# Kernel tuning notes

Measured on AMD Instinct MI355X. Metric: run time of the kernel, lower is better.

Reference implementation:

```python
import jax, jax.numpy as jnp
import numpy as np

B, N, E = 2, 16384, 262144          # batch, nodes, directed edges (avg deg 16)
K, D, Wm = 256, 3, 1                # nmodes, ndims, nmeasures
C, L, FC = 128, 4, 128              # channels, Fourier layers, fc hidden
IN_DIM, OUT_DIM = 3, 1


def setup_inputs() -> dict:
    key = jax.random.key(0)
    ks = jax.random.split(key, 20)
    s = 1.0 / (C * C)
    inp = {
        "x": jax.random.normal(ks[0], (B, N, IN_DIM), jnp.float32),
        "nodes": jax.random.uniform(ks[1], (B, N, D), jnp.float32),
        "node_mask": jnp.ones((B, N, 1), jnp.float32),
        "node_weights": jax.random.uniform(ks[2], (B, N, Wm), jnp.float32) / N,
        "directed_edges": jax.random.randint(ks[3], (B, E, 2), 0, N),
        "edge_gradient_weights": jax.random.normal(ks[4], (B, E, D), jnp.float32),
        "modes": jax.random.normal(ks[5], (K, D, Wm), jnp.float32),
        "sp_L": jnp.ones((D, Wm), jnp.float32),
        "weights_c": s * jax.random.uniform(ks[6], (L, C, C, K, Wm), jnp.float32),
        "weights_s": s * jax.random.uniform(ks[7], (L, C, C, K, Wm), jnp.float32),
        "weights_0": s * jax.random.uniform(ks[8], (L, C, C, 1, Wm), jnp.float32),
        "fc0_w": jax.random.normal(ks[9], (C, IN_DIM), jnp.float32) * 0.1,
        "fc0_b": jnp.zeros((C,), jnp.float32),
        "ws_w": jax.random.normal(ks[10], (L, C, C), jnp.float32) * 0.05,
        "ws_b": jnp.zeros((L, C), jnp.float32),
        "gws_w": jax.random.normal(ks[11], (L, C, D * C), jnp.float32) * 0.05,
        "gws_b": jnp.zeros((L, C), jnp.float32),
        "fc1_w": jax.random.normal(ks[12], (FC, C), jnp.float32) * 0.05,
        "fc1_b": jnp.zeros((FC,), jnp.float32),
        "fc2_w": jax.random.normal(ks[13], (OUT_DIM, FC), jnp.float32) * 0.05,
        "fc2_b": jnp.zeros((OUT_DIM,), jnp.float32),
    }
    return inp


def _gelu(x):
    return jax.nn.gelu(x, approximate=False)  # torch F.gelu default = exact erf


def _compute_gradient(f, directed_edges, edge_gradient_weights):
    # f: [B, C, N] -> gradients [B, C*D, N] via directed-edge scatter-add
    fT = jnp.transpose(f, (0, 2, 1))                       # [B, N, C]
    tgt, src = directed_edges[..., 0], directed_edges[..., 1]
    f_src = jnp.take_along_axis(fT, src[..., None], axis=1)  # [B, E, C]
    f_tgt = jnp.take_along_axis(fT, tgt[..., None], axis=1)
    msg = jnp.einsum('bed,bec->becd', edge_gradient_weights, f_src - f_tgt)
    msg = msg.reshape(msg.shape[0], msg.shape[1], -1)        # [B, E, C*D]

    def scat(m, t):
        return jnp.zeros((fT.shape[1], m.shape[-1]), m.dtype).at[t].add(m)

    g = jax.vmap(scat)(msg, tgt)                             # [B, N, C*D]
    return jnp.transpose(g, (0, 2, 1))


def _spectral_conv(x, wc, wsn, w0, bc, bs, b0, wbc, wbs, wb0):
    # x: [B, C_in, N]
    xc = jnp.einsum('bix,bxkw->bikw', x, wbc)
    xs = -jnp.einsum('bix,bxkw->bikw', x, wbs)
    x0 = jnp.einsum('bix,bxkw->bikw', x, wb0)
    fc = jnp.einsum('bikw,iokw->bokw', xc, wc) - jnp.einsum('bikw,iokw->bokw', xs, wsn)
    fs = jnp.einsum('bikw,iokw->bokw', xs, wc) + jnp.einsum('bikw,iokw->bokw', xc, wsn)
    f0 = jnp.einsum('bikw,iokw->bokw', x0, w0)
    return (jnp.einsum('bokw,bxkw->box', f0, b0)
            + 2.0 * jnp.einsum('bokw,bxkw->box', fc, bc)
            - 2.0 * jnp.einsum('bokw,bxkw->box', fs, bs))


def reference(x, nodes, node_mask, node_weights, directed_edges, edge_gradient_weights,
              modes, sp_L, weights_c, weights_s, weights_0,
              fc0_w, fc0_b, ws_w, ws_b, gws_w, gws_b, fc1_w, fc1_b, fc2_w, fc2_b):
    # Fourier bases with learnable length-scale sp_L: [K,D,Wm]*[D,Wm]
    temp = jnp.einsum('bxd,kdw->bxkw', nodes, modes * sp_L)   # [B,N,K,Wm]
    bc, bs = jnp.cos(temp), jnp.sin(temp)
    b0 = jnp.zeros((temp.shape[0], temp.shape[1], 1, temp.shape[3]), temp.dtype)
    nw = (node_weights * node_mask)[:, :, None, :]            # [B,N,1,Wm]
    wbc, wbs, wb0 = bc * nw, bs * nw, b0 * nw

    h = jnp.einsum('bxi,ci->bxc', x, fc0_w) + fc0_b           # lift [B,N,C]
    h = jnp.transpose(h, (0, 2, 1))                           # [B,C,N]

    for i in range(L):
        x1 = _spectral_conv(h, weights_c[i], weights_s[i], weights_0[i],
                            bc, bs, b0, wbc, wbs, wb0)
        x2 = jnp.einsum('oc,bcn->bon', ws_w[i], h) + ws_b[i][None, :, None]
        grad = _compute_gradient(h, directed_edges, edge_gradient_weights)
        x3 = jnp.einsum('og,bgn->bon', gws_w[i], grad) + gws_b[i][None, :, None]
        h = x1 + x2 + x3
        if i != L - 1:
            h = _gelu(h)

    h = jnp.transpose(h, (0, 2, 1))                           # [B,N,C]
    h = _gelu(jnp.einsum('bnc,fc->bnf', h, fc1_w) + fc1_b)
    out = jnp.einsum('bnf,of->bno', h, fc2_w) + fc2_b         # [B,N,out_dim]
    return out
```

## Files before the change

kernel.cpp:

```cpp
#include <hip/hip_runtime.h>
#include <math.h>

#define Bn 2
#define Nn 16384
#define En 262144
#define Kn 256
#define Cn 128
#define Rn 512
#define Ln 4
#define LDP 72
#define NSPLIT 64
#define MMSPLIT 4

typedef float f32x4 __attribute__((ext_vector_type(4)));
typedef short s16x8 __attribute__((ext_vector_type(8)));

__device__ __forceinline__ float gelu_f(float x){
  return 0.5f*x*(1.0f + erff(x*0.70710678118654752440f));
}
__device__ __forceinline__ unsigned short f2b(float x){
  unsigned int u = __float_as_uint(x);
  unsigned int r = (u + 0x7FFFu + ((u>>16)&1u)) >> 16;
  return (unsigned short)r;
}
__device__ __forceinline__ float b2f(unsigned short h){
  return __uint_as_float(((unsigned int)h)<<16);
}
__device__ __forceinline__ unsigned int pack2(float lo, float hi){
  return (unsigned int)f2b(lo) | ((unsigned int)f2b(hi) << 16);
}


__global__ __launch_bounds__(256) void k_nw(const float* __restrict__ nwt,
                                            const float* __restrict__ msk,
                                            float* __restrict__ nw){
  int i = blockIdx.x*256 + threadIdx.x;
  nw[i] = nwt[i]*msk[i];
}

__global__ __launch_bounds__(256) void k_basis(const float* __restrict__ nodes,
                                               const float* __restrict__ modes,
                                               const float* __restrict__ spl,
                                               unsigned short* __restrict__ basis,
                                               unsigned short* __restrict__ basisT){
  __shared__ unsigned short tile[32*520];
  int gn0 = blockIdx.x*32;
  int tid = threadIdx.x;
  float m0 = modes[tid*3+0]*spl[0];
  float m1 = modes[tid*3+1]*spl[1];
  float m2 = modes[tid*3+2]*spl[2];
  for (int j=0;j<32;j++){
    const float* nd = nodes + (size_t)(gn0+j)*3;
    float t = nd[0]*m0 + nd[1]*m1 + nd[2]*m2;
    float s,c;
    sincosf(t,&s,&c);
    tile[j*520 + tid]       = f2b(c);
    tile[j*520 + 256 + tid] = f2b(s);
  }
  __syncthreads();
  int row = tid>>3, col0 = (tid&7)*64;
  #pragma unroll
  for (int q=0;q<8;q++){
    s16x8 v = *(const s16x8*)&tile[row*520 + col0 + q*8];
    *(s16x8*)(basis + (size_t)(gn0+row)*Rn + col0 + q*8) = v;
  }
  int b = gn0 >> 14;
  int nl = gn0 & (Nn-1);
  #pragma unroll
  for (int h=0; h<2; h++){
    int r = h*256 + tid;
    unsigned short* dst = basisT + ((size_t)(b*Rn + r))*Nn + nl;
    #pragma unroll
    for (int q=0;q<4;q++){
      unsigned short tmp[8];
      #pragma unroll
      for (int e=0;e<8;e++) tmp[e] = tile[(q*8+e)*520 + r];
      *(s16x8*)(dst + q*8) = *(const s16x8*)tmp;
    }
  }
}

__global__ __launch_bounds__(256) void k_lift(const float* __restrict__ x,
                                              const float* __restrict__ w,
                                              const float* __restrict__ bias,
                                              const float* __restrict__ nw,
                                              unsigned short* __restrict__ hpack,
                                              unsigned short* __restrict__ hwT){
  __shared__ float ht[64*132];
  int gn0 = blockIdx.x*64;
  int tid = threadIdx.x;
  int c = tid & 127, rh = tid >> 7;
  float w0 = w[c*3], w1 = w[c*3+1], w2 = w[c*3+2], bb = bias[c];
  for (int j=0;j<32;j++){
    int n = rh*32 + j;
    const float* xp = x + (size_t)(gn0+n)*3;
    float v = bb + xp[0]*w0 + xp[1]*w1 + xp[2]*w2;
    ht[n*132 + c] = v;
    hpack[(size_t)(gn0+n)*Cn + c] = f2b(v);
  }
  __syncthreads();
  int b = gn0 >> 14, nl = gn0 & (Nn-1);
  int cc = tid>>1, hf = tid&1;
  unsigned short* dst = hwT + ((size_t)(b*Cn + cc))*Nn + nl + hf*32;
  #pragma unroll
  for (int q=0;q<8;q++){
    int n = hf*32 + q*4;
    float4 nv = *(const float4*)&nw[(size_t)b*Nn + nl + n];
    ushort4 pk;
    pk.x = f2b(ht[(n+0)*132+cc]*nv.x);
    pk.y = f2b(ht[(n+1)*132+cc]*nv.y);
    pk.z = f2b(ht[(n+2)*132+cc]*nv.z);
    pk.w = f2b(ht[(n+3)*132+cc]*nv.w);
    *(ushort4*)(dst + q*4) = pk;
  }
}

__global__ __launch_bounds__(128) void k_w2c(const float* __restrict__ ws_w,
                                             const float* __restrict__ ws_b,
                                             const float* __restrict__ gws_w,
                                             const float* __restrict__ gws_b,
                                             unsigned short* __restrict__ W2,
                                             float* __restrict__ bias2){
  int bid = blockIdx.x;
  int tid = threadIdx.x;
  unsigned short* wrow = W2 + (size_t)bid*Rn;
  wrow[tid] = f2b(ws_w[(size_t)bid*Cn + tid]);
  const float* g = gws_w + (size_t)bid*384;
  wrow[128+tid] = f2b(g[tid*3+0]);
  wrow[256+tid] = f2b(g[tid*3+1]);
  wrow[384+tid] = f2b(g[tid*3+2]);
  if (tid==0) bias2[bid] = ws_b[bid] + gws_b[bid];
}

__global__ __launch_bounds__(256) void k_cvt(const float* __restrict__ in,
                                             unsigned short* __restrict__ out, int n){
  int i = blockIdx.x*256 + threadIdx.x;
  if (i < n) out[i] = f2b(in[i]);
}


__global__ __launch_bounds__(256) void k_count(const int* __restrict__ de,
                                               int* __restrict__ cnt){
  int i = blockIdx.x*256 + threadIdx.x;
  int b = i >> 18;
  int tgt = de[(size_t)i*2];
  atomicAdd(&cnt[b*Nn + tgt], 1);
}

__global__ __launch_bounds__(1024) void k_scan(const int* __restrict__ cnt,
                                               int* __restrict__ rowptr,
                                               int* __restrict__ cursor){
  __shared__ int part[1024];
  int t = threadIdx.x;
  int b = t >> 9;
  int li = t & 511;
  int loc[32];
  int s = 0;
  int base = b*Nn + li*32;
  #pragma unroll
  for (int j=0;j<32;j++){ loc[j] = s; s += cnt[base+j]; }
  part[t] = s;
  __syncthreads();
  int run = s;
  for (int off=1; off<512; off<<=1){
    int v = (li >= off) ? part[t-off] : 0;
    __syncthreads();
    part[t] += v;
    __syncthreads();
  }
  int incl = part[t];
  int excl = incl - run;
  int rbase = b*(Nn+1) + li*32;
  #pragma unroll
  for (int j=0;j<32;j++){
    int val = excl + loc[j];
    rowptr[rbase+j] = val;
    cursor[base+j]  = val;
  }
  if (li == 511) rowptr[b*(Nn+1) + Nn] = incl;
}

__global__ __launch_bounds__(256) void k_fill(const int* __restrict__ de,
                                              const float* __restrict__ egw,
                                              int* __restrict__ cursor,
                                              float4* __restrict__ epack){
  int i = blockIdx.x*256 + threadIdx.x;
  int b = i >> 18;
  int tgt = de[(size_t)i*2];
  int src = de[(size_t)i*2+1];
  int pos = atomicAdd(&cursor[b*Nn + tgt], 1);
  const float* g = egw + (size_t)i*3;
  float4 pk;
  pk.x = __int_as_float(src);
  pk.y = g[0]; pk.z = g[1]; pk.w = g[2];
  epack[(size_t)b*En + pos] = pk;
}

__global__ __launch_bounds__(128) void k_grad(const unsigned short* __restrict__ hpack,
                                              const float4* __restrict__ epack,
                                              const int* __restrict__ rowptr,
                                              unsigned short* __restrict__ gradbuf){
  int bid = blockIdx.x;
  int b = bid >> 14, n = bid & (Nn-1);
  int tid = threadIdx.x;
  int wv = tid >> 6;
  int l  = tid & 63;
  const unsigned short* hb = hpack + (size_t)b*Nn*Cn;
  unsigned int ft2 = *(const unsigned int*)(hb + (size_t)n*Cn + 2*l);
  float ftlo = b2f((unsigned short)(ft2 & 0xffffu));
  float fthi = b2f((unsigned short)(ft2 >> 16));
  int beg = rowptr[b*(Nn+1) + n];
  int end = rowptr[b*(Nn+1) + n + 1];
  const float4* ep = epack + (size_t)b*En;
  float a0lo=0.f,a0hi=0.f,a1lo=0.f,a1hi=0.f,a2lo=0.f,a2hi=0.f;
  int j = beg + wv;
  for (; j + 6 < end; j += 8){
    float4 pk0 = ep[j];
    float4 pk1 = ep[j+2];
    float4 pk2 = ep[j+4];
    float4 pk3 = ep[j+6];
    unsigned int h0 = *(const unsigned int*)(hb + (size_t)__float_as_int(pk0.x)*Cn + 2*l);
    unsigned int h1 = *(const unsigned int*)(hb + (size_t)__float_as_int(pk1.x)*Cn + 2*l);
    unsigned int h2 = *(const unsigned int*)(hb + (size_t)__float_as_int(pk2.x)*Cn + 2*l);
    unsigned int h3 = *(const unsigned int*)(hb + (size_t)__float_as_int(pk3.x)*Cn + 2*l);
    float d0lo = b2f((unsigned short)(h0 & 0xffffu)) - ftlo;
    float d0hi = b2f((unsigned short)(h0 >> 16))     - fthi;
    float d1lo = b2f((unsigned short)(h1 & 0xffffu)) - ftlo;
    float d1hi = b2f((unsigned short)(h1 >> 16))     - fthi;
    float d2lo = b2f((unsigned short)(h2 & 0xffffu)) - ftlo;
    float d2hi = b2f((unsigned short)(h2 >> 16))     - fthi;
    float d3lo = b2f((unsigned short)(h3 & 0xffffu)) - ftlo;
    float d3hi = b2f((unsigned short)(h3 >> 16))     - fthi;
    a0lo += pk0.y*d0lo + pk1.y*d1lo + pk2.y*d2lo + pk3.y*d3lo;
    a0hi += pk0.y*d0hi + pk1.y*d1hi + pk2.y*d2hi + pk3.y*d3hi;
    a1lo += pk0.z*d0lo + pk1.z*d1lo + pk2.z*d2lo + pk3.z*d3lo;
    a1hi += pk0.z*d0hi + pk1.z*d1hi + pk2.z*d2hi + pk3.z*d3hi;
    a2lo += pk0.w*d0lo + pk1.w*d1lo + pk2.w*d2lo + pk3.w*d3lo;
    a2hi += pk0.w*d0hi + pk1.w*d1hi + pk2.w*d2hi + pk3.w*d3hi;
  }
  for (; j < end; j += 2){
    float4 pk = ep[j];
    int src = __float_as_int(pk.x);
    unsigned int hv = *(const unsigned int*)(hb + (size_t)src*Cn + 2*l);
    float dlo = b2f((unsigned short)(hv & 0xffffu)) - ftlo;
    float dhi = b2f((unsigned short)(hv >> 16))     - fthi;
    a0lo += pk.y*dlo; a0hi += pk.y*dhi;
    a1lo += pk.z*dlo; a1hi += pk.z*dhi;
    a2lo += pk.w*dlo; a2hi += pk.w*dhi;
  }
  __shared__ float red[64*7];
  if (wv == 1){
    float* r = &red[l*7];
    r[0]=a0lo; r[1]=a0hi; r[2]=a1lo; r[3]=a1hi; r[4]=a2lo; r[5]=a2hi;
  }
  __syncthreads();
  if (wv == 0){
    const float* r = &red[l*7];
    a0lo+=r[0]; a0hi+=r[1]; a1lo+=r[2]; a1hi+=r[3]; a2lo+=r[4]; a2hi+=r[5];
    unsigned short* o = gradbuf + ((size_t)b*Nn + n)*384;
    *(unsigned int*)(o + 2*l)       = pack2(a0lo, a0hi);
    *(unsigned int*)(o + 128 + 2*l) = pack2(a1lo, a1hi);
    *(unsigned int*)(o + 256 + 2*l) = pack2(a2lo, a2hi);
  }
}

__device__ __forceinline__ void stage_tile(const unsigned short* __restrict__ g, size_t ldg,
                                           unsigned short* __restrict__ lds, int tid){
  int row = tid >> 3;
  int seg = (tid & 7) * 8;
  #pragma unroll
  for (int rb=0; rb<4; rb++){
    s16x8 v = *(const s16x8*)(g + (size_t)(row + rb*32)*ldg + seg);
    *(s16x8*)(lds + (size_t)(row + rb*32)*LDP + seg) = v;
  }
}
__device__ __forceinline__ void stage_tile512(const unsigned short* __restrict__ g, size_t ldg,
                                              unsigned short* __restrict__ lds, int tid){
  int row = tid >> 3;
  int seg = (tid & 7) * 8;
  #pragma unroll
  for (int rb=0; rb<2; rb++){
    s16x8 v = *(const s16x8*)(g + (size_t)(row + rb*64)*ldg + seg);
    *(s16x8*)(lds + (size_t)(row + rb*64)*LDP + seg) = v;
  }
}

__device__ __forceinline__ void mfma_chunk(const unsigned short* __restrict__ As,
                                           const unsigned short* __restrict__ Bs,
                                           f32x4 acc[4][4], int wm, int wn, int lr, int lg){
  #pragma unroll
  for (int kk=0; kk<2; kk++){
    s16x8 a[4], b[4];
    #pragma unroll
    for (int i=0;i<4;i++)
      a[i] = *(const s16x8*)(As + (size_t)(wm*64 + i*16 + lr)*LDP + kk*32 + lg*8);
    #pragma unroll
    for (int i=0;i<4;i++)
      b[i] = *(const s16x8*)(Bs + (size_t)(wn*64 + i*16 + lr)*LDP + kk*32 + lg*8);
    #pragma unroll
    for (int i=0;i<4;i++)
      #pragma unroll
      for (int j=0;j<4;j++)
        acc[i][j] = __builtin_amdgcn_mfma_f32_16x16x32_bf16(a[i], b[j], acc[i][j], 0, 0, 0);
  }
}

__device__ __forceinline__ void mfma_chunk8(const unsigned short* __restrict__ As,
                                            const unsigned short* __restrict__ Bs,
                                            f32x4 acc[4][2], int wm, int wn, int lr, int lg){
  #pragma unroll
  for (int kk=0; kk<2; kk++){
    s16x8 a[4], b[2];
    #pragma unroll
    for (int i=0;i<4;i++)
      a[i] = *(const s16x8*)(As + (size_t)(wm*64 + i*16 + lr)*LDP + kk*32 + lg*8);
    #pragma unroll
    for (int j=0;j<2;j++)
      b[j] = *(const s16x8*)(Bs + (size_t)(wn*32 + j*16 + lr)*LDP + kk*32 + lg*8);
    #pragma unroll
    for (int i=0;i<4;i++)
      #pragma unroll
      for (int j=0;j<2;j++)
        acc[i][j] = __builtin_amdgcn_mfma_f32_16x16x32_bf16(a[i], b[j], acc[i][j], 0, 0, 0);
  }
}

__global__ __launch_bounds__(256) void k_fwd_mfma(const unsigned short* __restrict__ basisT,
                                                  const unsigned short* __restrict__ hwT,
                                                  float* __restrict__ part){
  __shared__ unsigned short As[128*LDP];
  __shared__ unsigned short Bs[128*LDP];
  int tid = threadIdx.x;
  int mt = blockIdx.x;
  int ks = blockIdx.y;
  int b  = blockIdx.z;
  const int KSP = Nn/NSPLIT;
  const unsigned short* A  = basisT + ((size_t)(b*Rn + mt*128))*Nn + (size_t)ks*KSP;
  const unsigned short* Bp = hwT   + ((size_t)(b*Cn))*Nn + (size_t)ks*KSP;
  f32x4 acc[4][4] = {};
  int l = tid & 63, w = tid >> 6, wm = w >> 1, wn = w & 1, lr = l & 15, lg = l >> 4;
  for (int k0 = 0; k0 < KSP; k0 += 64){
    stage_tile(A + k0, Nn, As, tid);
    stage_tile(Bp + k0, Nn, Bs, tid);
    __syncthreads();
    mfma_chunk(As, Bs, acc, wm, wn, lr, lg);
    __syncthreads();
  }
  float* pb = part + ((size_t)ks*Bn + b)*(Cn*Rn);
  int r0 = mt*128 + wm*64;
  int c0 = wn*64;
  #pragma unroll
  for (int i=0;i<4;i++)
    #pragma unroll
    for (int j=0;j<4;j++){
      int r = r0 + i*16 + lg*4;
      int c = c0 + j*16 + lr;
      *(f32x4*)&pb[(size_t)c*Rn + r] = acc[i][j];
    }
}

__global__ __launch_bounds__(256) void k_reduce(const float* __restrict__ part,
                                                float* __restrict__ xf){
  int idx = blockIdx.x*256 + threadIdx.x;
  float s = 0.f;
  #pragma unroll 8
  for (int ks=0; ks<NSPLIT; ks++)
    s += part[(size_t)ks*(Bn*Cn*Rn) + idx];
  xf[idx] = s;
}

__global__ __launch_bounds__(256) void k_mm(const float* __restrict__ xf,
                                            const float* __restrict__ wc,
                                            const float* __restrict__ ws,
                                            float* __restrict__ Fpart){
  int o  = blockIdx.x;
  int is = blockIdx.y;
  int tid = threadIdx.x;
  int g = tid >> 6;
  int l = tid & 63;
  int t4 = l*4;
  f32x4 fc0={},fs0={},fc1={},fs1={};
  #pragma unroll
  for (int ii=0; ii<8; ii++){
    int i = is*32 + g*8 + ii;
    f32x4 wc4 = *(const f32x4*)&wc[((size_t)i*Cn + o)*Kn + t4];
    f32x4 ws4 = *(const f32x4*)&ws[((size_t)i*Cn + o)*Kn + t4];
    f32x4 x0c = *(const f32x4*)&xf[(size_t)i*Rn + t4];
    f32x4 x0s = *(const f32x4*)&xf[(size_t)i*Rn + 256 + t4];
    f32x4 x1c = *(const f32x4*)&xf[(size_t)Cn*Rn + (size_t)i*Rn + t4];
    f32x4 x1s = *(const f32x4*)&xf[(size_t)Cn*Rn + (size_t)i*Rn + 256 + t4];
    fc0 += x0c*wc4 + x0s*ws4;  fs0 += x0c*ws4 - x0s*wc4;
    fc1 += x1c*wc4 + x1s*ws4;  fs1 += x1c*ws4 - x1s*wc4;
  }
  __shared__ float red[3][64][16];
  if (g > 0){
    float* r = red[g-1][l];
    *(f32x4*)&r[0]  = fc0;  *(f32x4*)&r[4]  = fs0;
    *(f32x4*)&r[8]  = fc1;  *(f32x4*)&r[12] = fs1;
  }
  __syncthreads();
  if (g == 0){
    #pragma unroll
    for (int q=0;q<3;q++){
      const float* r = red[q][l];
      fc0 += *(const f32x4*)&r[0];   fs0 += *(const f32x4*)&r[4];
      fc1 += *(const f32x4*)&r[8];   fs1 += *(const f32x4*)&r[12];
    }
    float* f0 = Fpart + ((size_t)(is*Bn + 0)*Cn + o)*Rn;
    float* f1 = Fpart + ((size_t)(is*Bn + 1)*Cn + o)*Rn;
    *(f32x4*)&f0[t4]       = fc0;
    *(f32x4*)&f0[256 + t4] = fs0;
    *(f32x4*)&f1[t4]       = fc1;
    *(f32x4*)&f1[256 + t4] = fs1;
  }
}

__global__ __launch_bounds__(256) void k_fcvt(const float* __restrict__ Fpart,
                                              unsigned short* __restrict__ Fbf){
  int idx = blockIdx.x*256 + threadIdx.x;
  float s = 0.f;
  #pragma unroll
  for (int q=0;q<MMSPLIT;q++)
    s += Fpart[(size_t)q*Bn*Cn*Rn + idx];
  float sc = ((idx & 511) < 256) ? 2.f : -2.f;
  Fbf[idx] = f2b(sc*s);
}

template<int GELU, int WRITE_AUX>
__global__ __launch_bounds__(512) void k_invcomb(const unsigned short* __restrict__ basis,
                                                 const unsigned short* __restrict__ Fbf,
                                                 const unsigned short* __restrict__ gradbuf,
                                                 const unsigned short* __restrict__ W2l,
                                                 const float* __restrict__ bias2l,
                                                 const float* __restrict__ nw,
                                                 unsigned short* __restrict__ hpack,
                                                 unsigned short* __restrict__ hwT){
  __shared__ unsigned short As1[128*LDP];
  __shared__ unsigned short Bs1[128*LDP];
  __shared__ unsigned short As2[128*LDP];
  __shared__ unsigned short Bs2[128*LDP];
  int tid = threadIdx.x;
  int nt = blockIdx.x;
  int b  = blockIdx.y;
  size_t nbase = (size_t)b*Nn + (size_t)nt*128;
  f32x4 acc[4][2] = {};
  int l = tid & 63, w = tid >> 6, wm = w >> 2, wn = w & 3, lr = l & 15, lg = l >> 4;
  const unsigned short* A1 = basis + nbase*Rn;
  const unsigned short* B1 = Fbf + (size_t)b*Cn*Rn;
  for (int k0=0;k0<512;k0+=64){
    stage_tile512(A1+k0, Rn, As1, tid);
    stage_tile512(B1+k0, Rn, Bs1, tid);
    if (k0 < 128) stage_tile512(hpack + nbase*Cn + k0, Cn, As2, tid);
    else          stage_tile512(gradbuf + nbase*384 + (k0-128), 384, As2, tid);
    stage_tile512(W2l+k0, Rn, Bs2, tid);
    __syncthreads();
    mfma_chunk8(As1,Bs1,acc,wm,wn,lr,lg);
    mfma_chunk8(As2,Bs2,acc,wm,wn,lr,lg);
    __syncthreads();
  }
  #pragma unroll
  for (int i=0;i<4;i++){
    int nloc = wm*64 + i*16 + lg*4;
    float4 w4;
    if (WRITE_AUX) w4 = *(const float4*)&nw[(size_t)b*Nn + nt*128 + nloc];
    #pragma unroll
    for (int j=0;j<2;j++){
      int c = wn*32 + j*16 + lr;
      float bsv = bias2l[c];
      float v[4];
      #pragma unroll
      for (int e=0;e<4;e++){
        v[e] = acc[i][j][e] + bsv;
        if (GELU) v[e] = gelu_f(v[e]);
        hpack[(nbase + nloc + e)*Cn + c] = f2b(v[e]);
      }
      if (WRITE_AUX){
        ushort4 pk;
        pk.x = f2b(v[0]*w4.x); pk.y = f2b(v[1]*w4.y);
        pk.z = f2b(v[2]*w4.z); pk.w = f2b(v[3]*w4.w);
        *(ushort4*)&hwT[((size_t)(b*Cn + c))*Nn + nt*128 + nloc] = pk;
      }
    }
  }
}

__global__ __launch_bounds__(512) void k_fc1(const unsigned short* __restrict__ hpack,
                                             const unsigned short* __restrict__ fw,
                                             const float* __restrict__ fb,
                                             unsigned short* __restrict__ h2){
  __shared__ unsigned short As[128*LDP];
  __shared__ unsigned short Bs[128*LDP];
  int tid = threadIdx.x;
  int nt = blockIdx.x;
  int b  = blockIdx.y;
  size_t nbase = (size_t)b*Nn + (size_t)nt*128;
  f32x4 acc[4][2] = {};
  int l = tid & 63, w = tid >> 6, wm = w >> 2, wn = w & 3, lr = l & 15, lg = l >> 4;
  const unsigned short* A = hpack + nbase*Cn;
  for (int k0=0;k0<128;k0+=64){
    stage_tile512(A+k0, Cn, As, tid);
    stage_tile512(fw+k0, Cn, Bs, tid);
    __syncthreads();
    mfma_chunk8(As,Bs,acc,wm,wn,lr,lg);
    __syncthreads();
  }
  #pragma unroll
  for (int i=0;i<4;i++){
    int nloc = wm*64 + i*16 + lg*4;
    #pragma unroll
    for (int j=0;j<2;j++){
      int c = wn*32 + j*16 + lr;
      float bsv = fb[c];
      #pragma unroll
      for (int e=0;e<4;e++){
        float v = gelu_f(acc[i][j][e] + bsv);
        h2[(nbase + nloc + e)*Cn + c] = f2b(v);
      }
    }
  }
}

__global__ __launch_bounds__(256) void k_out(const unsigned short* __restrict__ h2,
                                             const float* __restrict__ w,
                                             const float* __restrict__ bptr,
                                             float* __restrict__ outp){
  int tid = threadIdx.x;
  int node = blockIdx.x*4 + (tid>>6);
  int f = tid & 63;
  const unsigned short* hp = h2 + (size_t)node*Cn;
  float s = b2f(hp[f])*w[f] + b2f(hp[f+64])*w[f+64];
  #pragma unroll
  for (int off=32; off>0; off>>=1) s += __shfl_down(s, off);
  if (f==0) outp[node] = s + bptr[0];
}

static constexpr size_t OB_BASIS  = 0;
static constexpr size_t OB_BASIST = OB_BASIS  + 33554432;
static constexpr size_t OB_GRAD   = OB_BASIST + 33554432;
static constexpr size_t OB_HWT    = OB_GRAD   + 25165824;
static constexpr size_t OB_H2     = OB_HWT    + 8388608;
static constexpr size_t OB_HP     = OB_H2     + 8388608;
static constexpr size_t OB_NW     = OB_HP     + 8388608;
static constexpr size_t OB_XF     = OB_NW     + 131072;
static constexpr size_t OB_FBF    = OB_XF     + 524288;
static constexpr size_t OB_FPART  = OB_FBF    + 262144;
static constexpr size_t OB_W2     = OB_FPART  + 2097152;
static constexpr size_t OB_B2     = OB_W2     + 524288;
static constexpr size_t OB_FC1W   = OB_B2     + 2048;
static constexpr size_t OB_EPACK  = OB_FC1W   + 32768;
static constexpr size_t OB_INT    = OB_EPACK  + 8388608;
static constexpr size_t OB_PART   = OB_INT    + 524288;

extern "C" void kernel_launch(void* const* d_in, const int* in_sizes, int n_in,
                              void* d_out, int out_size, void* d_ws, size_t ws_size,
                              hipStream_t stream) {
  const float* x            = (const float*)d_in[0];
  const float* nodes        = (const float*)d_in[1];
  const float* node_mask    = (const float*)d_in[2];
  const float* node_weights = (const float*)d_in[3];
  const int*   de           = (const int*)  d_in[4];
  const float* egw          = (const float*)d_in[5];
  const float* modes        = (const float*)d_in[6];
  const float* spl          = (const float*)d_in[7];
  const float* wc           = (const float*)d_in[8];
  const float* wsp          = (const float*)d_in[9];
  const float* fc0_w        = (const float*)d_in[11];
  const float* fc0_b        = (const float*)d_in[12];
  const float* ws_w         = (const float*)d_in[13];
  const float* ws_b         = (const float*)d_in[14];
  const float* gws_w        = (const float*)d_in[15];
  const float* gws_b        = (const float*)d_in[16];
  const float* fc1_w        = (const float*)d_in[17];
  const float* fc1_b        = (const float*)d_in[18];
  const float* fc2_w        = (const float*)d_in[19];
  const float* fc2_b        = (const float*)d_in[20];
  float* outp = (float*)d_out;

  char* wsb = (char*)d_ws;
  unsigned short* basis   = (unsigned short*)(wsb + OB_BASIS);
  unsigned short* basisT  = (unsigned short*)(wsb + OB_BASIST);
  unsigned short* gradbuf = (unsigned short*)(wsb + OB_GRAD);
  unsigned short* hwT     = (unsigned short*)(wsb + OB_HWT);
  unsigned short* h2      = (unsigned short*)(wsb + OB_H2);
  unsigned short* hpack   = (unsigned short*)(wsb + OB_HP);
  float* nw               = (float*)(wsb + OB_NW);
  float* xf               = (float*)(wsb + OB_XF);
  unsigned short* Fbf     = (unsigned short*)(wsb + OB_FBF);
  float* Fpart            = (float*)(wsb + OB_FPART);
  unsigned short* W2      = (unsigned short*)(wsb + OB_W2);
  float* bias2            = (float*)(wsb + OB_B2);
  unsigned short* fc1wb   = (unsigned short*)(wsb + OB_FC1W);
  float4* epack           = (float4*)(wsb + OB_EPACK);
  int* count  = (int*)(wsb + OB_INT);
  int* rowptr = count + Bn*Nn;
  int* cursor = rowptr + Bn*(Nn+1);
  float* part = (float*)(wsb + OB_PART);

  k_nw<<<(Bn*Nn)/256, 256, 0, stream>>>(node_weights, node_mask, nw);
  k_basis<<<(Bn*Nn)/32, 256, 0, stream>>>(nodes, modes, spl, basis, basisT);
  k_lift<<<(Bn*Nn)/64, 256, 0, stream>>>(x, fc0_w, fc0_b, nw, hpack, hwT);

  (void)hipMemsetAsync(count, 0, (size_t)Bn*Nn*sizeof(int), stream);
  k_count<<<(Bn*En)/256, 256, 0, stream>>>(de, count);
  k_scan<<<1, 1024, 0, stream>>>(count, rowptr, cursor);
  k_fill<<<(Bn*En)/256, 256, 0, stream>>>(de, egw, cursor, epack);

  k_w2c<<<Ln*Cn, 128, 0, stream>>>(ws_w, ws_b, gws_w, gws_b, W2, bias2);
  k_cvt<<<64, 256, 0, stream>>>(fc1_w, fc1wb, Cn*Cn);

  for (int l=0; l<Ln; l++){
    k_fwd_mfma<<<dim3(4,NSPLIT,2), 256, 0, stream>>>(basisT, hwT, part);
    k_reduce<<<(Bn*Cn*Rn)/256, 256, 0, stream>>>(part, xf);
    k_mm<<<dim3(Cn,MMSPLIT), 256, 0, stream>>>(xf, wc + (size_t)l*Cn*Cn*Kn,
                                               wsp + (size_t)l*Cn*Cn*Kn, Fpart);
    k_fcvt<<<(Bn*Cn*Rn)/256, 256, 0, stream>>>(Fpart, Fbf);
    k_grad<<<Bn*Nn, 128, 0, stream>>>(hpack, epack, rowptr, gradbuf);
    if (l < Ln-1){
      k_invcomb<1,1><<<dim3(Nn/128,2), 512, 0, stream>>>(
          basis, Fbf, gradbuf, W2 + (size_t)l*Cn*Rn, bias2 + l*Cn, nw, hpack, hwT);
    } else {
      k_invcomb<0,0><<<dim3(Nn/128,2), 512, 0, stream>>>(
          basis, Fbf, gradbuf, W2 + (size_t)l*Cn*Rn, bias2 + l*Cn, nw, hpack, hwT);
    }
  }

  k_fc1<<<dim3(Nn/128,2), 512, 0, stream>>>(hpack, fc1wb, fc1_b, h2);
  k_out<<<(Bn*Nn)/4, 256, 0, stream>>>(h2, fc2_w, fc2_b, outp);
}
```

Baseline: 511.7 us.

## Store split-K partials in bf16 and fuse spectral matmul with gradient kernel

The forward split-K GEMM now writes its partial sums as bf16 instead of fp32, and the reduce kernel reads packed pairs, roughly halving partial-buffer traffic. The spectral weight matmul and the edge-gradient scatter are merged into one launch: the first blocks run the matmul, and the rest process two nodes per 256-thread block for the gradient. This removes a kernel launch and lets the two independent stages overlap on the device. The cost is extra rounding error from bf16 partials summed over 64 splits.

```diff
diff --git a/kernel.cpp b/kernel.cpp
--- a/kernel.cpp
+++ b/kernel.cpp
@@ -11,6 +11,7 @@
 #define LDP 72
 #define NSPLIT 64
 #define MMSPLIT 4
+#define MMB (Cn*MMSPLIT)
 
 typedef float f32x4 __attribute__((ext_vector_type(4)));
 typedef short s16x8 __attribute__((ext_vector_type(8)));
@@ -196,15 +197,177 @@
   epack[(size_t)b*En + pos] = pk;
 }
 
-__global__ __launch_bounds__(128) void k_grad(const unsigned short* __restrict__ hpack,
-                                              const float4* __restrict__ epack,
-                                              const int* __restrict__ rowptr,
-                                              unsigned short* __restrict__ gradbuf){
+__device__ __forceinline__ void stage_tile(const unsigned short* __restrict__ g, size_t ldg,
+                                           unsigned short* __restrict__ lds, int tid){
+  int row = tid >> 3;
+  int seg = (tid & 7) * 8;
+  #pragma unroll
+  for (int rb=0; rb<4; rb++){
+    s16x8 v = *(const s16x8*)(g + (size_t)(row + rb*32)*ldg + seg);
+    *(s16x8*)(lds + (size_t)(row + rb*32)*LDP + seg) = v;
+  }
+}
+__device__ __forceinline__ void stage_tile512(const unsigned short* __restrict__ g, size_t ldg,
+                                              unsigned short* __restrict__ lds, int tid){
+  int row = tid >> 3;
+  int seg = (tid & 7) * 8;
+  #pragma unroll
+  for (int rb=0; rb<2; rb++){
+    s16x8 v = *(const s16x8*)(g + (size_t)(row + rb*64)*ldg + seg);
+    *(s16x8*)(lds + (size_t)(row + rb*64)*LDP + seg) = v;
+  }
+}
+
+__device__ __forceinline__ void mfma_chunk(const unsigned short* __restrict__ As,
+                                           const unsigned short* __restrict__ Bs,
+                                           f32x4 acc[4][4], int wm, int wn, int lr, int lg){
+  #pragma unroll
+  for (int kk=0; kk<2; kk++){
+    s16x8 a[4], b[4];
+    #pragma unroll
+    for (int i=0;i<4;i++)
+      a[i] = *(const s16x8*)(As + (size_t)(wm*64 + i*16 + lr)*LDP + kk*32 + lg*8);
+    #pragma unroll
+    for (int i=0;i<4;i++)
+      b[i] = *(const s16x8*)(Bs + (size_t)(wn*64 + i*16 + lr)*LDP + kk*32 + lg*8);
+    #pragma unroll
+    for (int i=0;i<4;i++)
+      #pragma unroll
+      for (int j=0;j<4;j++)
+        acc[i][j] = __builtin_amdgcn_mfma_f32_16x16x32_bf16(a[i], b[j], acc[i][j], 0, 0, 0);
+  }
+}
+
+__device__ __forceinline__ void mfma_chunk8(const unsigned short* __restrict__ As,
+                                            const unsigned short* __restrict__ Bs,
+                                            f32x4 acc[4][2], int wm, int wn, int lr, int lg){
+  #pragma unroll
+  for (int kk=0; kk<2; kk++){
+    s16x8 a[4], b[2];
+    #pragma unroll
+    for (int i=0;i<4;i++)
+      a[i] = *(const s16x8*)(As + (size_t)(wm*64 + i*16 + lr)*LDP + kk*32 + lg*8);
+    #pragma unroll
+    for (int j=0;j<2;j++)
+      b[j] = *(const s16x8*)(Bs + (size_t)(wn*32 + j*16 + lr)*LDP + kk*32 + lg*8);
+    #pragma unroll
+    for (int i=0;i<4;i++)
+      #pragma unroll
+      for (int j=0;j<2;j++)
+        acc[i][j] = __builtin_amdgcn_mfma_f32_16x16x32_bf16(a[i], b[j], acc[i][j], 0, 0, 0);
+  }
+}
+
+__global__ __launch_bounds__(256) void k_fwd_mfma(const unsigned short* __restrict__ basisT,
+                                                  const unsigned short* __restrict__ hwT,
+                                                  unsigned short* __restrict__ part16){
+  __shared__ unsigned short As[128*LDP];
+  __shared__ unsigned short Bs[128*LDP];
+  int tid = threadIdx.x;
+  int mt = blockIdx.x;
+  int ks = blockIdx.y;
+  int b  = blockIdx.z;
+  const int KSP = Nn/NSPLIT;
+  const unsigned short* A  = basisT + ((size_t)(b*Rn + mt*128))*Nn + (size_t)ks*KSP;
+  const unsigned short* Bp = hwT   + ((size_t)(b*Cn))*Nn + (size_t)ks*KSP;
+  f32x4 acc[4][4] = {};
+  int l = tid & 63, w = tid >> 6, wm = w >> 1, wn = w & 1, lr = l & 15, lg = l >> 4;
+  for (int k0 = 0; k0 < KSP; k0 += 64){
+    stage_tile(A + k0, Nn, As, tid);
+    stage_tile(Bp + k0, Nn, Bs, tid);
+    __syncthreads();
+    mfma_chunk(As, Bs, acc, wm, wn, lr, lg);
+    __syncthreads();
+  }
+  unsigned short* pb = part16 + ((size_t)ks*Bn + b)*(Cn*Rn);
+  int r0 = mt*128 + wm*64;
+  int c0 = wn*64;
+  #pragma unroll
+  for (int i=0;i<4;i++)
+    #pragma unroll
+    for (int j=0;j<4;j++){
+      int r = r0 + i*16 + lg*4;
+      int c = c0 + j*16 + lr;
+      unsigned short* p = pb + (size_t)c*Rn + r;
+      *(unsigned int*)(p)     = pack2(acc[i][j][0], acc[i][j][1]);
+      *(unsigned int*)(p + 2) = pack2(acc[i][j][2], acc[i][j][3]);
+    }
+}
+
+__global__ __launch_bounds__(256) void k_reduce(const unsigned int* __restrict__ part32,
+                                                float* __restrict__ xf){
+  int idx = blockIdx.x*256 + threadIdx.x;
+  const int STRIDE = Bn*Cn*Rn/2;
+  float s0 = 0.f, s1 = 0.f;
+  #pragma unroll 8
+  for (int ks=0; ks<NSPLIT; ks++){
+    unsigned int v = part32[(size_t)ks*STRIDE + idx];
+    s0 += b2f((unsigned short)(v & 0xffffu));
+    s1 += b2f((unsigned short)(v >> 16));
+  }
+  float2 o; o.x = s0; o.y = s1;
+  *(float2*)&xf[(size_t)idx*2] = o;
+}
+
+__global__ __launch_bounds__(256) void k_mmgrad(const float* __restrict__ xf,
+                                                const float* __restrict__ wc,
+                                                const float* __restrict__ ws,
+                                                float* __restrict__ Fpart,
+                                                const unsigned short* __restrict__ hpack,
+                                                const float4* __restrict__ epack,
+                                                const int* __restrict__ rowptr,
+                                                unsigned short* __restrict__ gradbuf){
+  __shared__ float smem[3072];
   int bid = blockIdx.x;
-  int b = bid >> 14, n = bid & (Nn-1);
-  int tid = threadIdx.x;
-  int wv = tid >> 6;
+  int tid = threadIdx.x;
+  if (bid < MMB){
+    int o  = bid & 127;
+    int is = bid >> 7;
+    int g = tid >> 6;
+    int l = tid & 63;
+    int t4 = l*4;
+    f32x4 fc0={},fs0={},fc1={},fs1={};
+    #pragma unroll
+    for (int ii=0; ii<8; ii++){
+      int i = is*32 + g*8 + ii;
+      f32x4 wc4 = *(const f32x4*)&wc[((size_t)i*Cn + o)*Kn + t4];
+      f32x4 ws4 = *(const f32x4*)&ws[((size_t)i*Cn + o)*Kn + t4];
+      f32x4 x0c = *(const f32x4*)&xf[(size_t)i*Rn + t4];
+      f32x4 x0s = *(const f32x4*)&xf[(size_t)i*Rn + 256 + t4];
+      f32x4 x1c = *(const f32x4*)&xf[(size_t)Cn*Rn + (size_t)i*Rn + t4];
+      f32x4 x1s = *(const f32x4*)&xf[(size_t)Cn*Rn + (size_t)i*Rn + 256 + t4];
+      fc0 += x0c*wc4 + x0s*ws4;  fs0 += x0c*ws4 - x0s*wc4;
+      fc1 += x1c*wc4 + x1s*ws4;  fs1 += x1c*ws4 - x1s*wc4;
+    }
+    float (*red)[64][16] = (float(*)[64][16])smem;
+    if (g > 0){
+      float* r = red[g-1][l];
+      *(f32x4*)&r[0]  = fc0;  *(f32x4*)&r[4]  = fs0;
+      *(f32x4*)&r[8]  = fc1;  *(f32x4*)&r[12] = fs1;
+    }
+    __syncthreads();
+    if (g == 0){
+      #pragma unroll
+      for (int q=0;q<3;q++){
+        const float* r = red[q][l];
+        fc0 += *(const f32x4*)&r[0];   fs0 += *(const f32x4*)&r[4];
+        fc1 += *(const f32x4*)&r[8];   fs1 += *(const f32x4*)&r[12];
+      }
+      float* f0 = Fpart + ((size_t)(is*Bn + 0)*Cn + o)*Rn;
+      float* f1 = Fpart + ((size_t)(is*Bn + 1)*Cn + o)*Rn;
+      *(f32x4*)&f0[t4]       = fc0;
+      *(f32x4*)&f0[256 + t4] = fs0;
+      *(f32x4*)&f1[t4]       = fc1;
+      *(f32x4*)&f1[256 + t4] = fs1;
+    }
+    return;
+  }
+  int gg = bid - MMB;
+  int b = gg >> 13;
+  int n = ((gg & 8191) << 1) | (tid >> 7);
+  int wv = (tid >> 6) & 1;
   int l  = tid & 63;
+  int half = tid >> 7;
   const unsigned short* hb = hpack + (size_t)b*Nn*Cn;
   unsigned int ft2 = *(const unsigned int*)(hb + (size_t)n*Cn + 2*l);
   float ftlo = b2f((unsigned short)(ft2 & 0xffffu));
@@ -248,170 +411,18 @@
     a1lo += pk.z*dlo; a1hi += pk.z*dhi;
     a2lo += pk.w*dlo; a2hi += pk.w*dhi;
   }
-  __shared__ float red[64*7];
   if (wv == 1){
-    float* r = &red[l*7];
+    float* r = &smem[(half*64 + l)*7];
     r[0]=a0lo; r[1]=a0hi; r[2]=a1lo; r[3]=a1hi; r[4]=a2lo; r[5]=a2hi;
   }
   __syncthreads();
   if (wv == 0){
-    const float* r = &red[l*7];
+    const float* r = &smem[(half*64 + l)*7];
     a0lo+=r[0]; a0hi+=r[1]; a1lo+=r[2]; a1hi+=r[3]; a2lo+=r[4]; a2hi+=r[5];
     unsigned short* o = gradbuf + ((size_t)b*Nn + n)*384;
     *(unsigned int*)(o + 2*l)       = pack2(a0lo, a0hi);
     *(unsigned int*)(o + 128 + 2*l) = pack2(a1lo, a1hi);
     *(unsigned int*)(o + 256 + 2*l) = pack2(a2lo, a2hi);
-  }
-}
-
-__device__ __forceinline__ void stage_tile(const unsigned short* __restrict__ g, size_t ldg,
-                                           unsigned short* __restrict__ lds, int tid){
-  int row = tid >> 3;
-  int seg = (tid & 7) * 8;
-  #pragma unroll
-  for (int rb=0; rb<4; rb++){
-    s16x8 v = *(const s16x8*)(g + (size_t)(row + rb*32)*ldg + seg);
-    *(s16x8*)(lds + (size_t)(row + rb*32)*LDP + seg) = v;
-  }
-}
-__device__ __forceinline__ void stage_tile512(const unsigned short* __restrict__ g, size_t ldg,
-                                              unsigned short* __restrict__ lds, int tid){
-  int row = tid >> 3;
-  int seg = (tid & 7) * 8;
-  #pragma unroll
-  for (int rb=0; rb<2; rb++){
-    s16x8 v = *(const s16x8*)(g + (size_t)(row + rb*64)*ldg + seg);
-    *(s16x8*)(lds + (size_t)(row + rb*64)*LDP + seg) = v;
-  }
-}
-
-__device__ __forceinline__ void mfma_chunk(const unsigned short* __restrict__ As,
-                                           const unsigned short* __restrict__ Bs,
-                                           f32x4 acc[4][4], int wm, int wn, int lr, int lg){
-  #pragma unroll
-  for (int kk=0; kk<2; kk++){
-    s16x8 a[4], b[4];
-    #pragma unroll
-    for (int i=0;i<4;i++)
-      a[i] = *(const s16x8*)(As + (size_t)(wm*64 + i*16 + lr)*LDP + kk*32 + lg*8);
-    #pragma unroll
-    for (int i=0;i<4;i++)
-      b[i] = *(const s16x8*)(Bs + (size_t)(wn*64 + i*16 + lr)*LDP + kk*32 + lg*8);
-    #pragma unroll
-    for (int i=0;i<4;i++)
-      #pragma unroll
-      for (int j=0;j<4;j++)
-        acc[i][j] = __builtin_amdgcn_mfma_f32_16x16x32_bf16(a[i], b[j], acc[i][j], 0, 0, 0);
-  }
-}
-
-__device__ __forceinline__ void mfma_chunk8(const unsigned short* __restrict__ As,
-                                            const unsigned short* __restrict__ Bs,
-                                            f32x4 acc[4][2], int wm, int wn, int lr, int lg){
-  #pragma unroll
-  for (int kk=0; kk<2; kk++){
-    s16x8 a[4], b[2];
-    #pragma unroll
-    for (int i=0;i<4;i++)
-      a[i] = *(const s16x8*)(As + (size_t)(wm*64 + i*16 + lr)*LDP + kk*32 + lg*8);
-    #pragma unroll
-    for (int j=0;j<2;j++)
-      b[j] = *(const s16x8*)(Bs + (size_t)(wn*32 + j*16 + lr)*LDP + kk*32 + lg*8);
-    #pragma unroll
-    for (int i=0;i<4;i++)
-      #pragma unroll
-      for (int j=0;j<2;j++)
-        acc[i][j] = __builtin_amdgcn_mfma_f32_16x16x32_bf16(a[i], b[j], acc[i][j], 0, 0, 0);
-  }
-}
-
-__global__ __launch_bounds__(256) void k_fwd_mfma(const unsigned short* __restrict__ basisT,
-                                                  const unsigned short* __restrict__ hwT,
-                                                  float* __restrict__ part){
-  __shared__ unsigned short As[128*LDP];
-  __shared__ unsigned short Bs[128*LDP];
-  int tid = threadIdx.x;
-  int mt = blockIdx.x;
-  int ks = blockIdx.y;
-  int b  = blockIdx.z;
-  const int KSP = Nn/NSPLIT;
-  const unsigned short* A  = basisT + ((size_t)(b*Rn + mt*128))*Nn + (size_t)ks*KSP;
-  const unsigned short* Bp = hwT   + ((size_t)(b*Cn))*Nn + (size_t)ks*KSP;
-  f32x4 acc[4][4] = {};
-  int l = tid & 63, w = tid >> 6, wm = w >> 1, wn = w & 1, lr = l & 15, lg = l >> 4;
-  for (int k0 = 0; k0 < KSP; k0 += 64){
-    stage_tile(A + k0, Nn, As, tid);
-    stage_tile(Bp + k0, Nn, Bs, tid);
-    __syncthreads();
-    mfma_chunk(As, Bs, acc, wm, wn, lr, lg);
-    __syncthreads();
-  }
-  float* pb = part + ((size_t)ks*Bn + b)*(Cn*Rn);
-  int r0 = mt*128 + wm*64;
-  int c0 = wn*64;
-  #pragma unroll
-  for (int i=0;i<4;i++)
-    #pragma unroll
-    for (int j=0;j<4;j++){
-      int r = r0 + i*16 + lg*4;
-      int c = c0 + j*16 + lr;
-      *(f32x4*)&pb[(size_t)c*Rn + r] = acc[i][j];
-    }
-}
-
-__global__ __launch_bounds__(256) void k_reduce(const float* __restrict__ part,
-                                                float* __restrict__ xf){
-  int idx = blockIdx.x*256 + threadIdx.x;
-  float s = 0.f;
-  #pragma unroll 8
-  for (int ks=0; ks<NSPLIT; ks++)
-    s += part[(size_t)ks*(Bn*Cn*Rn) + idx];
-  xf[idx] = s;
-}
-
-__global__ __launch_bounds__(256) void k_mm(const float* __restrict__ xf,
-                                            const float* __restrict__ wc,
-                                            const float* __restrict__ ws,
-                                            float* __restrict__ Fpart){
-  int o  = blockIdx.x;
-  int is = blockIdx.y;
-  int tid = threadIdx.x;
-  int g = tid >> 6;
-  int l = tid & 63;
-  int t4 = l*4;
-  f32x4 fc0={},fs0={},fc1={},fs1={};
-  #pragma unroll
-  for (int ii=0; ii<8; ii++){
-    int i = is*32 + g*8 + ii;
-    f32x4 wc4 = *(const f32x4*)&wc[((size_t)i*Cn + o)*Kn + t4];
-    f32x4 ws4 = *(const f32x4*)&ws[((size_t)i*Cn + o)*Kn + t4];
-    f32x4 x0c = *(const f32x4*)&xf[(size_t)i*Rn + t4];
-    f32x4 x0s = *(const f32x4*)&xf[(size_t)i*Rn + 256 + t4];
-    f32x4 x1c = *(const f32x4*)&xf[(size_t)Cn*Rn + (size_t)i*Rn + t4];
-    f32x4 x1s = *(const f32x4*)&xf[(size_t)Cn*Rn + (size_t)i*Rn + 256 + t4];
-    fc0 += x0c*wc4 + x0s*ws4;  fs0 += x0c*ws4 - x0s*wc4;
-    fc1 += x1c*wc4 + x1s*ws4;  fs1 += x1c*ws4 - x1s*wc4;
-  }
-  __shared__ float red[3][64][16];
-  if (g > 0){
-    float* r = red[g-1][l];
-    *(f32x4*)&r[0]  = fc0;  *(f32x4*)&r[4]  = fs0;
-    *(f32x4*)&r[8]  = fc1;  *(f32x4*)&r[12] = fs1;
-  }
-  __syncthreads();
-  if (g == 0){
-    #pragma unroll
-    for (int q=0;q<3;q++){
-      const float* r = red[q][l];
-      fc0 += *(const f32x4*)&r[0];   fs0 += *(const f32x4*)&r[4];
-      fc1 += *(const f32x4*)&r[8];   fs1 += *(const f32x4*)&r[12];
-    }
-    float* f0 = Fpart + ((size_t)(is*Bn + 0)*Cn + o)*Rn;
-    float* f1 = Fpart + ((size_t)(is*Bn + 1)*Cn + o)*Rn;
-    *(f32x4*)&f0[t4]       = fc0;
-    *(f32x4*)&f0[256 + t4] = fs0;
-    *(f32x4*)&f1[t4]       = fc1;
-    *(f32x4*)&f1[256 + t4] = fs1;
   }
 }
 
@@ -594,7 +605,7 @@
   int* count  = (int*)(wsb + OB_INT);
   int* rowptr = count + Bn*Nn;
   int* cursor = rowptr + Bn*(Nn+1);
-  float* part = (float*)(wsb + OB_PART);
+  unsigned short* part16 = (unsigned short*)(wsb + OB_PART);
 
   k_nw<<<(Bn*Nn)/256, 256, 0, stream>>>(node_weights, node_mask, nw);
   k_basis<<<(Bn*Nn)/32, 256, 0, stream>>>(nodes, modes, spl, basis, basisT);
@@ -609,12 +620,12 @@
   k_cvt<<<64, 256, 0, stream>>>(fc1_w, fc1wb, Cn*Cn);
 
   for (int l=0; l<Ln; l++){
-    k_fwd_mfma<<<dim3(4,NSPLIT,2), 256, 0, stream>>>(basisT, hwT, part);
-    k_reduce<<<(Bn*Cn*Rn)/256, 256, 0, stream>>>(part, xf);
-    k_mm<<<dim3(Cn,MMSPLIT), 256, 0, stream>>>(xf, wc + (size_t)l*Cn*Cn*Kn,
-                                               wsp + (size_t)l*Cn*Cn*Kn, Fpart);
+    k_fwd_mfma<<<dim3(4,NSPLIT,2), 256, 0, stream>>>(basisT, hwT, part16);
+    k_reduce<<<(Bn*Cn*Rn/2)/256, 256, 0, stream>>>((const unsigned int*)part16, xf);
+    k_mmgrad<<<MMB + (Bn*Nn)/2, 256, 0, stream>>>(xf, wc + (size_t)l*Cn*Cn*Kn,
+                                                  wsp + (size_t)l*Cn*Cn*Kn, Fpart,
+                                                  hpack, epack, rowptr, gradbuf);
     k_fcvt<<<(Bn*Cn*Rn)/256, 256, 0, stream>>>(Fpart, Fbf);
-    k_grad<<<Bn*Nn, 128, 0, stream>>>(hpack, epack, rowptr, gradbuf);
     if (l < Ln-1){
       k_invcomb<1,1><<<dim3(Nn/128,2), 512, 0, stream>>>(
           basis, Fbf, gradbuf, W2 + (size_t)l*Cn*Rn, bias2 + l*Cn, nw, hpack, hwT);
```

Result: no change. 517.1 us (+1.0%).
